# Optimization experiments

Measured on AMD Instinct MI355X. Metric: run time of the kernel, lower is better.

Reference implementation:

```python
import jax, jax.numpy as jnp
import numpy as np

N, H, E, K, C, M = 4096, 512, 512, 64, 128, 4  # tokens, hidden, embed, categories, children/cat, max_num_children
IN = E + H  # LSTMCell input size


def setup_inputs() -> dict:
    key = jax.random.key(0)
    ks = jax.random.split(key, 12)
    s = 0.05
    return {
        "et": jax.random.normal(ks[0], (N, H), jnp.float32),
        "x": jax.random.normal(ks[1], (N, IN), jnp.float32),
        "h": jax.random.normal(ks[2], (N, H), jnp.float32),
        "c": jax.random.normal(ks[3], (N, H), jnp.float32),
        "cat": jax.random.randint(ks[4], (N,), 0, K, jnp.int32),
        "ci": jax.random.randint(ks[5], (N,), 0, M, jnp.int32),
        # per-category prediction Linear(hidden_size -> |children(category)|)
        "W_lin": jax.random.normal(ks[6], (K, C, H), jnp.float32) * s,
        "b_lin": jax.random.normal(ks[7], (K, C), jnp.float32) * s,
        # per-child-index LSTMCell(embedding+hidden -> hidden), torch gate order i,f,g,o
        "W_ih": jax.random.normal(ks[8], (M, 4 * H, IN), jnp.float32) * s,
        "W_hh": jax.random.normal(ks[9], (M, 4 * H, H), jnp.float32) * s,
        "b_ih": jax.random.normal(ks[10], (M, 4 * H), jnp.float32) * s,
        "b_hh": jax.random.normal(ks[11], (M, 4 * H), jnp.float32) * s,
    }


def reference(et, x, h, c, cat, ci, W_lin, b_lin, W_ih, W_hh, b_ih, b_hh):
    # get_log_odds: route each token to its category's Linear (gather weights, per-token matvec)
    Wg = W_lin[cat]                                   # [N, C, H]
    log_odds = jnp.einsum('nh,nch->nc', et, Wg) + b_lin[cat]  # [N, C]

    # get_next: LSTMCell selected by child_index. Only M=4 cells, so compute all
    # cells' gates densely (efficient GEMMs) and select with a one-hot mix.
    gates_all = (jnp.einsum('ni,kgi->nkg', x, W_ih)
                 + jnp.einsum('nh,kgh->nkg', h, W_hh)
                 + (b_ih + b_hh)[None])               # [N, M, 4H]
    sel = jax.nn.one_hot(ci, M, dtype=gates_all.dtype)  # [N, M]
    gates = jnp.einsum('nkg,nk->ng', gates_all, sel)     # [N, 4H]
    i_, f_, g_, o_ = jnp.split(gates, 4, axis=-1)
    c2 = jax.nn.sigmoid(f_) * c + jax.nn.sigmoid(i_) * jnp.tanh(g_)
    h2 = jax.nn.sigmoid(o_) * jnp.tanh(c2)
    return log_odds, h2, c2
```

## Files before the change

kernel.cpp:

```cpp
#include <hip/hip_runtime.h>
#include <hip/hip_bf16.h>
#include <stdint.h>

#define NTOK 4096
#define HID  512
#define INSZ 1024
#define KIN  1536
#define KSEG 768
#define KCAT 64
#define CCH  128
#define MCELL 4
#define G4H  2048

typedef unsigned short u16;
typedef __bf16 bf16x8 __attribute__((ext_vector_type(8)));
typedef float  f32x4  __attribute__((ext_vector_type(4)));

__device__ __forceinline__ u16 f2bf(float f) {
    unsigned u = __float_as_uint(f);
    u += 0x7fffu + ((u >> 16) & 1u);
    return (u16)(u >> 16);
}
__device__ __forceinline__ float bf2f(u16 v) {
    return __uint_as_float(((unsigned)v) << 16);
}
__device__ __forceinline__ void store_bf4(u16* p, float4 v) {
    ushort4 r;
    r.x = f2bf(v.x); r.y = f2bf(v.y); r.z = f2bf(v.z); r.w = f2bf(v.w);
    *reinterpret_cast<ushort4*>(p) = r;
}
__device__ __forceinline__ void gl16(const u16* g, u16* l) {
    __builtin_amdgcn_global_load_lds((const __attribute__((address_space(1))) void*)g,
                                     (__attribute__((address_space(3))) void*)l, 16, 0, 0);
}

#define P0_W 8192
#define P0_L 2731
__global__ __launch_bounds__(192) void pack_all(
    const float* __restrict__ Wih, const float* __restrict__ Whh,
    const float* __restrict__ W_lin,
    const int* __restrict__ ci, const int* __restrict__ cat,
    u16* __restrict__ Wb, u16* __restrict__ Wlin,
    int* __restrict__ meta, int* __restrict__ perm_ci, int* __restrict__ perm_cat)
{
    int b = blockIdx.x;
    int tid = threadIdx.x;
    int c = tid * 8;
    if (b < P0_W) {
        int m = b >> 11, j = b & 2047;
        const float* src = (c < INSZ) ? (Wih + ((size_t)m * G4H + j) * INSZ + c)
                                      : (Whh + ((size_t)m * G4H + j) * HID + (c - INSZ));
        u16* dst = Wb + (size_t)b * KIN + c;
        store_bf4(dst, *(const float4*)src);
        store_bf4(dst + 4, *(const float4*)(src + 4));
    } else if (b < P0_W + P0_L) {
        int row = (b - P0_W) * 3 + (c >> 9);
        int col = c & 511;
        if (row >= KCAT * CCH) return;
        const float* src = W_lin + (size_t)row * HID + col;
        u16* dst = Wlin + (size_t)row * HID + col;
        store_bf4(dst, *(const float4*)src);
        store_bf4(dst + 4, *(const float4*)(src + 4));
    } else {
        __shared__ int cnt_ci[MCELL], cur_ci[MCELL];
        __shared__ int cnt_cat[KCAT], cur_cat[KCAT];
        if (tid < MCELL) cnt_ci[tid] = 0;
        if (tid < KCAT)  cnt_cat[tid] = 0;
        __syncthreads();
        for (int t = tid; t < NTOK; t += 192) {
            atomicAdd(&cnt_ci[ci[t]], 1);
            atomicAdd(&cnt_cat[cat[t]], 1);
        }
        __syncthreads();
        if (tid == 0) {
            int off = 0;
            for (int m = 0; m < MCELL; ++m) {
                int p = (cnt_ci[m] + 127) & ~127;
                meta[m] = p; meta[4 + m] = off; cur_ci[m] = off; off += p;
            }
            off = 0;
            for (int i = 0; i < 128; ++i) meta[136 + i] = -1;
            for (int k = 0; k < KCAT; ++k) {
                int p = (cnt_cat[k] + 63) & ~63;
                meta[8 + k] = p; meta[72 + k] = off; cur_cat[k] = off;
                for (int i = 0; i < p / 64; ++i) meta[136 + off / 64 + i] = k;
                off += p;
            }
        }
        __syncthreads();
        for (int i = tid; i < 4608; i += 192) perm_ci[i] = -1;
        for (int i = tid; i < 8192; i += 192) perm_cat[i] = -1;
        __syncthreads();
        for (int t = tid; t < NTOK; t += 192) {
            int s = atomicAdd(&cur_ci[ci[t]], 1);
            perm_ci[s] = t;
            int sc = atomicAdd(&cur_cat[cat[t]], 1);
            perm_cat[sc] = t;
        }
    }
}

__global__ __launch_bounds__(192) void pack_slots(
    const float* __restrict__ x, const float* __restrict__ h,
    const int* __restrict__ perm_ci,
    u16* __restrict__ A_pack, int* __restrict__ inv_ci)
{
    int b = blockIdx.x;
    int tid = threadIdx.x;
    int c = tid * 8;
    int t = perm_ci[b];
    if (tid == 0 && t >= 0) inv_ci[t] = b;
    u16* dst = A_pack + (size_t)b * KIN + c;
    if (t < 0) {
        *reinterpret_cast<int4*>(dst) = make_int4(0, 0, 0, 0);
        return;
    }
    const float* src = (c < INSZ) ? (x + (size_t)t * INSZ + c)
                                  : (h + (size_t)t * HID + (c - INSZ));
    store_bf4(dst, *(const float4*)src);
    store_bf4(dst + 4, *(const float4*)(src + 4));
}

__global__ __launch_bounds__(256, 4) void mega_gemm(
    const u16* __restrict__ A_pack,
    const u16* __restrict__ Wb,
    const u16* __restrict__ Wlin,
    const float* __restrict__ et,
    const float* __restrict__ b_lin,
    const int* __restrict__ meta,
    const int* __restrict__ perm_cat,
    u16* __restrict__ gates0,
    u16* __restrict__ gates1,
    float* __restrict__ out)
{
    __shared__ __align__(16) u16 As[8192];
    __shared__ __align__(16) u16 Bs[8192];
    __shared__ int sperm[64];

    int tid = threadIdx.x;
    int lane = tid & 63, wave = tid >> 6;
    int rb = tid >> 3;
    int kc = (tid & 7) ^ (rb & 7);
    int qd = lane >> 4, l15 = lane & 15;
    int rsw = l15 & 7;

    int id = blockIdx.x;
    if (id < 4608) {
        int g = id & 63;
        int r = id >> 6;
        int m = g >> 4, ct = g & 15;
        int seg = r & 1, rt = r >> 1;
        int pcnt = meta[m];
        if (rt * 128 >= pcnt) return;
        int row0 = meta[4 + m] + rt * 128;
        int k0 = seg * KSEG;

        const u16* gA[4]; const u16* gB[4];
        u16* lA[4]; u16* lB[4];
        #pragma unroll
        for (int i = 0; i < 4; ++i) {
            gA[i] = A_pack + (size_t)(row0 + i * 32 + rb) * KIN + k0 + kc * 8;
            gB[i] = Wb + ((size_t)m * G4H + ct * 128 + i * 32 + rb) * KIN + k0 + kc * 8;
            lA[i] = As + (i * 256 + wave * 64) * 8;
            lB[i] = Bs + (i * 256 + wave * 64) * 8;
        }

        int wr = wave >> 1, wc = wave & 1;

        f32x4 acc[4][4];
        #pragma unroll
        for (int i = 0; i < 4; ++i)
            #pragma unroll
            for (int j = 0; j < 4; ++j)
                acc[i][j] = (f32x4){0.f, 0.f, 0.f, 0.f};

        for (int ks = 0; ks < KSEG / 64; ++ks) {
            #pragma unroll
            for (int i = 0; i < 4; ++i) { gl16(gA[i], lA[i]); gl16(gB[i], lB[i]); }
            #pragma unroll
            for (int i = 0; i < 4; ++i) { gA[i] += 64; gB[i] += 64; }
            __syncthreads();
            #pragma unroll
            for (int ks2 = 0; ks2 < 2; ++ks2) {
                bf16x8 fa[4], fb[4];
                #pragma unroll
                for (int ti = 0; ti < 4; ++ti) {
                    int row = wr * 64 + ti * 16 + l15;
                    int ch = (ks2 * 4 + qd) ^ rsw;
                    fa[ti] = *reinterpret_cast<const bf16x8*>(&As[row * 64 + ch * 8]);
                }
                #pragma unroll
                for (int tj = 0; tj < 4; ++tj) {
                    int row = wc * 64 + tj * 16 + l15;
                    int ch = (ks2 * 4 + qd) ^ rsw;
                    fb[tj] = *reinterpret_cast<const bf16x8*>(&Bs[row * 64 + ch * 8]);
                }
                #pragma unroll
                for (int ti = 0; ti < 4; ++ti)
                    #pragma unroll
                    for (int tj = 0; tj < 4; ++tj)
                        acc[ti][tj] = __builtin_amdgcn_mfma_f32_16x16x32_bf16(fa[ti], fb[tj], acc[ti][tj], 0, 0, 0);
            }
            __syncthreads();
        }

        u16* gout = seg ? gates1 : gates0;
        #pragma unroll
        for (int ti = 0; ti < 4; ++ti) {
            #pragma unroll
            for (int tj = 0; tj < 4; ++tj) {
                int gcol = ct * 128 + wc * 64 + tj * 16 + l15;
                #pragma unroll
                for (int rr = 0; rr < 4; ++rr) {
                    int grow = row0 + wr * 64 + ti * 16 + qd * 4 + rr;
                    gout[(size_t)grow * G4H + gcol] = f2bf(acc[ti][tj][rr]);
                }
            }
        }
    } else {
        int rtl = id - 4608;
        int k = meta[136 + rtl];
        if (k < 0) return;
        int r0 = rtl * 64;

        if (tid < 64) sperm[tid] = perm_cat[r0 + tid];
        __syncthreads();

        const u16* gW[4]; u16* lW[4];
        #pragma unroll
        for (int i = 0; i < 4; ++i) {
            gW[i] = Wlin + ((size_t)k * CCH + i * 32 + rb) * HID + kc * 8;
            lW[i] = As + (i * 256 + wave * 64) * 8;
        }
        int ar = tid >> 2;
        int acp = tid & 3;
        int at = sperm[ar];
        const float* asrc = (at >= 0) ? (et + (size_t)at * HID) : nullptr;

        f32x4 acc[4][2];
        #pragma unroll
        for (int i = 0; i < 4; ++i) {
            acc[i][0] = (f32x4){0.f, 0.f, 0.f, 0.f};
            acc[i][1] = (f32x4){0.f, 0.f, 0.f, 0.f};
        }

        for (int kk = 0; kk < HID; kk += 64) {
            #pragma unroll
            for (int i = 0; i < 4; ++i) { gl16(gW[i], lW[i]); gW[i] += 64; }
            #pragma unroll
            for (int j = 0; j < 2; ++j) {
                int dch = acp * 2 + j;
                int sch = dch ^ (ar & 7);
                u16* dst = &Bs[ar * 64 + dch * 8];
                if (asrc) {
                    const float* s = asrc + kk + sch * 8;
                    store_bf4(dst,     *(const float4*)s);
                    store_bf4(dst + 4, *(const float4*)(s + 4));
                } else {
                    *reinterpret_cast<int4*>(dst) = make_int4(0, 0, 0, 0);
                }
            }
            __syncthreads();
            #pragma unroll
            for (int ks2 = 0; ks2 < 2; ++ks2) {
                bf16x8 fa[4], fb[2];
                #pragma unroll
                for (int ti = 0; ti < 4; ++ti) {
                    int row = ti * 16 + l15;
                    int ch = (ks2 * 4 + qd) ^ rsw;
                    fa[ti] = *reinterpret_cast<const bf16x8*>(&Bs[row * 64 + ch * 8]);
                }
                #pragma unroll
                for (int tj = 0; tj < 2; ++tj) {
                    int row = wave * 32 + tj * 16 + l15;
                    int ch = (ks2 * 4 + qd) ^ rsw;
                    fb[tj] = *reinterpret_cast<const bf16x8*>(&As[row * 64 + ch * 8]);
                }
                #pragma unroll
                for (int ti = 0; ti < 4; ++ti)
                    #pragma unroll
                    for (int tj = 0; tj < 2; ++tj)
                        acc[ti][tj] = __builtin_amdgcn_mfma_f32_16x16x32_bf16(fa[ti], fb[tj], acc[ti][tj], 0, 0, 0);
            }
            __syncthreads();
        }

        #pragma unroll
        for (int ti = 0; ti < 4; ++ti) {
            #pragma unroll
            for (int tj = 0; tj < 2; ++tj) {
                int n = wave * 32 + tj * 16 + l15;
                float bias = b_lin[k * CCH + n];
                #pragma unroll
                for (int rr = 0; rr < 4; ++rr) {
                    int row = ti * 16 + qd * 4 + rr;
                    int t = sperm[row];
                    if (t >= 0)
                        out[(size_t)t * CCH + n] = acc[ti][tj][rr] + bias;
                }
            }
        }
    }
}

__global__ __launch_bounds__(256) void lstm_epilogue(
    const u16* __restrict__ gates0, const u16* __restrict__ gates1,
    const int* __restrict__ meta,
    const int* __restrict__ inv_ci,
    const float* __restrict__ c,
    const float* __restrict__ b_ih,
    const float* __restrict__ b_hh,
    float* __restrict__ out)
{
    int idx = blockIdx.x * 256 + threadIdx.x;
    int t = idx >> 9;
    int hh = idx & 511;
    int s = inv_ci[t];
    int m = (s >= meta[5]) + (s >= meta[6]) + (s >= meta[7]);

    const u16* g0 = gates0 + (size_t)s * G4H;
    const u16* g1 = gates1 + (size_t)s * G4H;
    const float* bi = b_ih + (size_t)m * G4H;
    const float* bh = b_hh + (size_t)m * G4H;
    float gi = bf2f(g0[hh])        + bf2f(g1[hh])        + bi[hh]        + bh[hh];
    float gf = bf2f(g0[512 + hh])  + bf2f(g1[512 + hh])  + bi[512 + hh]  + bh[512 + hh];
    float gg = bf2f(g0[1024 + hh]) + bf2f(g1[1024 + hh]) + bi[1024 + hh] + bh[1024 + hh];
    float go = bf2f(g0[1536 + hh]) + bf2f(g1[1536 + hh]) + bi[1536 + hh] + bh[1536 + hh];

    float si = 1.f / (1.f + __expf(-gi));
    float sf = 1.f / (1.f + __expf(-gf));
    float so = 1.f / (1.f + __expf(-go));
    float ct = c[(size_t)t * HID + hh];
    float c2 = sf * ct + si * tanhf(gg);
    float h2 = so * tanhf(c2);

    const size_t o_h2 = (size_t)NTOK * CCH;
    const size_t o_c2 = o_h2 + (size_t)NTOK * HID;
    out[o_h2 + (size_t)t * HID + hh] = h2;
    out[o_c2 + (size_t)t * HID + hh] = c2;
}

extern "C" void kernel_launch(void* const* d_in, const int* in_sizes, int n_in,
                              void* d_out, int out_size, void* d_ws, size_t ws_size,
                              hipStream_t stream) {
    const float* et    = (const float*)d_in[0];
    const float* x     = (const float*)d_in[1];
    const float* h     = (const float*)d_in[2];
    const float* c     = (const float*)d_in[3];
    const int*   cat   = (const int*)d_in[4];
    const int*   ci    = (const int*)d_in[5];
    const float* W_lin = (const float*)d_in[6];
    const float* b_lin = (const float*)d_in[7];
    const float* W_ih  = (const float*)d_in[8];
    const float* W_hh  = (const float*)d_in[9];
    const float* b_ih  = (const float*)d_in[10];
    const float* b_hh  = (const float*)d_in[11];
    float* out = (float*)d_out;

    char* ws = (char*)d_ws;
    int* meta     = (int*)ws;
    int* perm_ci  = (int*)(ws + 2048);
    int* perm_cat = (int*)(ws + 20480);
    int* inv_ci   = (int*)(ws + 53248);
    u16* A_pack   = (u16*)(ws + 69632);
    u16* Wb       = (u16*)(ws + 14225408);
    u16* Wlin     = (u16*)(ws + 39391232);
    u16* gates0   = (u16*)(ws + 47779840);
    u16* gates1   = (u16*)(ws + 66654208);

    pack_all<<<P0_W + P0_L + 1, 192, 0, stream>>>(W_ih, W_hh, W_lin, ci, cat,
                                                  Wb, Wlin, meta, perm_ci, perm_cat);

    pack_slots<<<4608, 192, 0, stream>>>(x, h, perm_ci, A_pack, inv_ci);

    mega_gemm<<<4608 + 128, 256, 0, stream>>>(A_pack, Wb, Wlin, et, b_lin, meta,
                                              perm_cat, gates0, gates1, out);

    lstm_epilogue<<<(NTOK * HID) / 256, 256, 0, stream>>>(gates0, gates1, meta,
                                                          inv_ci, c, b_ih, b_hh, out);
}
```

Baseline: 258.8 us.

## Split permutation build into its own kernel and merge all packing into one grid-stride kernel

Moves the token counting and permutation build out of the weight-pack kernel into a small single-block kernel with 1024 threads, which also writes inv_ci. Weight packing (W_ih/W_hh, W_lin) and activation slot packing are then merged into one grid-stride kernel over a fixed 2048 blocks. The aim is to stop the single serial permutation block from stretching the tail of the big pack launch and to cut the fine-grained 192-thread blocks down to fewer, fatter ones. The cost is that the small serial kernel now runs alone ahead of the pack, and the pack loop does integer divides per chunk.

```diff
diff --git a/kernel.cpp b/kernel.cpp
--- a/kernel.cpp
+++ b/kernel.cpp
@@ -24,101 +24,105 @@
 __device__ __forceinline__ float bf2f(u16 v) {
     return __uint_as_float(((unsigned)v) << 16);
 }
-__device__ __forceinline__ void store_bf4(u16* p, float4 v) {
-    ushort4 r;
-    r.x = f2bf(v.x); r.y = f2bf(v.y); r.z = f2bf(v.z); r.w = f2bf(v.w);
-    *reinterpret_cast<ushort4*>(p) = r;
+__device__ __forceinline__ void store_bf8(u16* p, float4 a, float4 b) {
+    ushort4 r0, r1;
+    r0.x = f2bf(a.x); r0.y = f2bf(a.y); r0.z = f2bf(a.z); r0.w = f2bf(a.w);
+    r1.x = f2bf(b.x); r1.y = f2bf(b.y); r1.z = f2bf(b.z); r1.w = f2bf(b.w);
+    *reinterpret_cast<ushort4*>(p) = r0;
+    *reinterpret_cast<ushort4*>(p + 4) = r1;
 }
 __device__ __forceinline__ void gl16(const u16* g, u16* l) {
     __builtin_amdgcn_global_load_lds((const __attribute__((address_space(1))) void*)g,
                                      (__attribute__((address_space(3))) void*)l, 16, 0, 0);
 }
 
-#define P0_W 8192
-#define P0_L 2731
-__global__ __launch_bounds__(192) void pack_all(
+__global__ __launch_bounds__(1024) void build_perm(
+    const int* __restrict__ ci, const int* __restrict__ cat,
+    int* __restrict__ meta, int* __restrict__ perm_ci,
+    int* __restrict__ inv_ci, int* __restrict__ perm_cat)
+{
+    __shared__ int cnt_ci[MCELL], cur_ci[MCELL];
+    __shared__ int cnt_cat[KCAT], cur_cat[KCAT];
+    int tid = threadIdx.x;
+    if (tid < MCELL) cnt_ci[tid] = 0;
+    if (tid < KCAT)  cnt_cat[tid] = 0;
+    __syncthreads();
+    for (int t = tid; t < NTOK; t += 1024) {
+        atomicAdd(&cnt_ci[ci[t]], 1);
+        atomicAdd(&cnt_cat[cat[t]], 1);
+    }
+    __syncthreads();
+    if (tid == 0) {
+        int off = 0;
+        for (int m = 0; m < MCELL; ++m) {
+            int p = (cnt_ci[m] + 127) & ~127;
+            meta[m] = p; meta[4 + m] = off; cur_ci[m] = off; off += p;
+        }
+        off = 0;
+        for (int i = 0; i < 128; ++i) meta[136 + i] = -1;
+        for (int k = 0; k < KCAT; ++k) {
+            int p = (cnt_cat[k] + 63) & ~63;
+            meta[8 + k] = p; meta[72 + k] = off; cur_cat[k] = off;
+            for (int i = 0; i < p / 64; ++i) meta[136 + off / 64 + i] = k;
+            off += p;
+        }
+    }
+    __syncthreads();
+    for (int i = tid; i < 4608; i += 1024) perm_ci[i] = -1;
+    for (int i = tid; i < 8192; i += 1024) perm_cat[i] = -1;
+    __syncthreads();
+    for (int t = tid; t < NTOK; t += 1024) {
+        int s = atomicAdd(&cur_ci[ci[t]], 1);
+        perm_ci[s] = t;
+        inv_ci[t] = s;
+        int sc = atomicAdd(&cur_cat[cat[t]], 1);
+        perm_cat[sc] = t;
+    }
+}
+
+#define CH_W  (8192 * 192)
+#define CH_L  (8192 * 64)
+#define CH_A  (4608 * 192)
+#define CH_TOT (CH_W + CH_L + CH_A)
+#define PK_BLOCKS 2048
+
+__global__ __launch_bounds__(256) void fat_pack(
+    const float* __restrict__ x, const float* __restrict__ h,
     const float* __restrict__ Wih, const float* __restrict__ Whh,
     const float* __restrict__ W_lin,
-    const int* __restrict__ ci, const int* __restrict__ cat,
-    u16* __restrict__ Wb, u16* __restrict__ Wlin,
-    int* __restrict__ meta, int* __restrict__ perm_ci, int* __restrict__ perm_cat)
+    const int* __restrict__ perm_ci,
+    u16* __restrict__ A_pack, u16* __restrict__ Wb, u16* __restrict__ Wlin)
 {
-    int b = blockIdx.x;
-    int tid = threadIdx.x;
-    int c = tid * 8;
-    if (b < P0_W) {
-        int m = b >> 11, j = b & 2047;
-        const float* src = (c < INSZ) ? (Wih + ((size_t)m * G4H + j) * INSZ + c)
-                                      : (Whh + ((size_t)m * G4H + j) * HID + (c - INSZ));
-        u16* dst = Wb + (size_t)b * KIN + c;
-        store_bf4(dst, *(const float4*)src);
-        store_bf4(dst + 4, *(const float4*)(src + 4));
-    } else if (b < P0_W + P0_L) {
-        int row = (b - P0_W) * 3 + (c >> 9);
-        int col = c & 511;
-        if (row >= KCAT * CCH) return;
-        const float* src = W_lin + (size_t)row * HID + col;
-        u16* dst = Wlin + (size_t)row * HID + col;
-        store_bf4(dst, *(const float4*)src);
-        store_bf4(dst + 4, *(const float4*)(src + 4));
-    } else {
-        __shared__ int cnt_ci[MCELL], cur_ci[MCELL];
-        __shared__ int cnt_cat[KCAT], cur_cat[KCAT];
-        if (tid < MCELL) cnt_ci[tid] = 0;
-        if (tid < KCAT)  cnt_cat[tid] = 0;
-        __syncthreads();
-        for (int t = tid; t < NTOK; t += 192) {
-            atomicAdd(&cnt_ci[ci[t]], 1);
-            atomicAdd(&cnt_cat[cat[t]], 1);
-        }
-        __syncthreads();
-        if (tid == 0) {
-            int off = 0;
-            for (int m = 0; m < MCELL; ++m) {
-                int p = (cnt_ci[m] + 127) & ~127;
-                meta[m] = p; meta[4 + m] = off; cur_ci[m] = off; off += p;
-            }
-            off = 0;
-            for (int i = 0; i < 128; ++i) meta[136 + i] = -1;
-            for (int k = 0; k < KCAT; ++k) {
-                int p = (cnt_cat[k] + 63) & ~63;
-                meta[8 + k] = p; meta[72 + k] = off; cur_cat[k] = off;
-                for (int i = 0; i < p / 64; ++i) meta[136 + off / 64 + i] = k;
-                off += p;
-            }
-        }
-        __syncthreads();
-        for (int i = tid; i < 4608; i += 192) perm_ci[i] = -1;
-        for (int i = tid; i < 8192; i += 192) perm_cat[i] = -1;
-        __syncthreads();
-        for (int t = tid; t < NTOK; t += 192) {
-            int s = atomicAdd(&cur_ci[ci[t]], 1);
-            perm_ci[s] = t;
-            int sc = atomicAdd(&cur_cat[cat[t]], 1);
-            perm_cat[sc] = t;
-        }
-    }
-}
-
-__global__ __launch_bounds__(192) void pack_slots(
-    const float* __restrict__ x, const float* __restrict__ h,
-    const int* __restrict__ perm_ci,
-    u16* __restrict__ A_pack, int* __restrict__ inv_ci)
-{
-    int b = blockIdx.x;
-    int tid = threadIdx.x;
-    int c = tid * 8;
-    int t = perm_ci[b];
-    if (tid == 0 && t >= 0) inv_ci[t] = b;
-    u16* dst = A_pack + (size_t)b * KIN + c;
-    if (t < 0) {
-        *reinterpret_cast<int4*>(dst) = make_int4(0, 0, 0, 0);
-        return;
-    }
-    const float* src = (c < INSZ) ? (x + (size_t)t * INSZ + c)
-                                  : (h + (size_t)t * HID + (c - INSZ));
-    store_bf4(dst, *(const float4*)src);
-    store_bf4(dst + 4, *(const float4*)(src + 4));
+    for (int i = blockIdx.x * 256 + threadIdx.x; i < CH_TOT; i += PK_BLOCKS * 256) {
+        if (i < CH_W) {
+            int row = i / 192, cc = i - row * 192;
+            int m = row >> 11, j = row & 2047;
+            int c = cc * 8;
+            const float* src = (c < INSZ) ? (Wih + ((size_t)m * G4H + j) * INSZ + c)
+                                          : (Whh + ((size_t)m * G4H + j) * HID + (c - INSZ));
+            store_bf8(Wb + (size_t)row * KIN + c,
+                      *(const float4*)src, *(const float4*)(src + 4));
+        } else if (i < CH_W + CH_L) {
+            int i2 = i - CH_W;
+            int row = i2 >> 6, cc = i2 & 63;
+            const float* src = W_lin + (size_t)row * HID + cc * 8;
+            store_bf8(Wlin + (size_t)row * HID + cc * 8,
+                      *(const float4*)src, *(const float4*)(src + 4));
+        } else {
+            int i3 = i - (CH_W + CH_L);
+            int row = i3 / 192, cc = i3 - row * 192;
+            int c = cc * 8;
+            u16* dst = A_pack + (size_t)row * KIN + c;
+            int t = perm_ci[row];
+            if (t < 0) {
+                *reinterpret_cast<int4*>(dst) = make_int4(0, 0, 0, 0);
+            } else {
+                const float* src = (c < INSZ) ? (x + (size_t)t * INSZ + c)
+                                              : (h + (size_t)t * HID + (c - INSZ));
+                store_bf8(dst, *(const float4*)src, *(const float4*)(src + 4));
+            }
+        }
+    }
 }
 
 __global__ __launch_bounds__(256, 4) void mega_gemm(
@@ -254,8 +258,7 @@
                 u16* dst = &Bs[ar * 64 + dch * 8];
                 if (asrc) {
                     const float* s = asrc + kk + sch * 8;
-                    store_bf4(dst,     *(const float4*)s);
-                    store_bf4(dst + 4, *(const float4*)(s + 4));
+                    store_bf8(dst, *(const float4*)s, *(const float4*)(s + 4));
                 } else {
                     *reinterpret_cast<int4*>(dst) = make_int4(0, 0, 0, 0);
                 }
@@ -368,10 +371,10 @@
     u16* gates0   = (u16*)(ws + 47779840);
     u16* gates1   = (u16*)(ws + 66654208);
 
-    pack_all<<<P0_W + P0_L + 1, 192, 0, stream>>>(W_ih, W_hh, W_lin, ci, cat,
-                                                  Wb, Wlin, meta, perm_ci, perm_cat);
-
-    pack_slots<<<4608, 192, 0, stream>>>(x, h, perm_ci, A_pack, inv_ci);
+    build_perm<<<1, 1024, 0, stream>>>(ci, cat, meta, perm_ci, inv_ci, perm_cat);
+
+    fat_pack<<<PK_BLOCKS, 256, 0, stream>>>(x, h, W_ih, W_hh, W_lin, perm_ci,
+                                            A_pack, Wb, Wlin);
 
     mega_gemm<<<4608 + 128, 256, 0, stream>>>(A_pack, Wb, Wlin, et, b_lin, meta,
                                               perm_cat, gates0, gates1, out);
```

After: 236.6 us. -8.6%, faster.
